# Performance work log

Measured on AMD Instinct MI355X. Metric: run time of the kernel, lower is better.

## Reference

```python
import jax, jax.numpy as jnp
import numpy as np

EPS = 1e-06
M = 10.0
IGNORE_LABEL = 100  # setup guarantees no label == 100, so the torch filter is a no-op


def setup_inputs() -> dict:
    key = jax.random.key(0)
    kf, kl = jax.random.split(key)
    n, d = 8192, 128
    features = jax.random.normal(kf, (n, d), dtype=jnp.float32)
    labels = jax.random.randint(kl, (n,), 0, 16, dtype=jnp.int64)
    return {"features": features, "labels": labels}


def reference(features, labels):
    # features: (n, d) float; labels: (n,) int, none equal to IGNORE_LABEL
    n = features.shape[0]
    dt = features.dtype

    # pairwise squared euclidean distances via Gram trick (avoids (n,n,d) tensor)
    sq = jnp.sum(features * features, axis=1)              # (n,)
    ed = sq[:, None] + sq[None, :] - 2.0 * (features @ features.T)  # (n, n)

    eq = labels[:, None] == labels[None, :]                # (n, n), includes diagonal
    counts = jnp.sum(eq, axis=1, keepdims=True).astype(dt) - 1.0  # (n, 1)

    eqf = eq.astype(dt)
    w = eqf / (counts + EPS) - (1.0 - eqf) / (n - counts - 1.0 + EPS)
    w = w * (1.0 - jnp.eye(n, dtype=dt))                   # zero diagonal

    loss = jnp.sum(w * ed, axis=1) + M                     # (n,)
    valid = (counts[:, 0] != 0.0).astype(dt)               # rows with same-class neighbors
    return jnp.sum(jax.nn.relu(loss) * valid) / jnp.maximum(jnp.sum(valid), 1.0)
```

## Files before the change

### kernel.cpp

```cpp
#include <hip/hip_runtime.h>

#define NCLASS 16
#define D 128
#define EPSF 1e-6f
#define MF 10.0f

#define WS_S   0
#define WS_Q   (NCLASS * D)
#define WS_CNT (WS_Q + NCLASS)
#define WS_SUM (WS_CNT + NCLASS)
#define WS_DONE 2082
#define WS_FLOATS 2084

#define AGG_BLOCKS 64
#define AGG_THREADS 512
#define AGG_WAVES (AGG_THREADS / 64)

__global__ void __launch_bounds__(AGG_THREADS)
agg_kernel(const float* __restrict__ F, const int* __restrict__ L,
           float* __restrict__ ws, int n) {
    __shared__ float Ssh[AGG_WAVES][NCLASS][D];
    __shared__ float qsh[AGG_WAVES][NCLASS];
    __shared__ float csh[AGG_WAVES][NCLASS];
    const int tid  = threadIdx.x;
    const int lane = tid & 63;
    const int wv   = tid >> 6;
    const int gw   = blockIdx.x * AGG_WAVES + wv;
    const int nwv  = AGG_BLOCKS * AGG_WAVES;

    float ax[NCLASS], ay[NCLASS], qa[NCLASS], ca[NCLASS];
    #pragma unroll
    for (int c = 0; c < NCLASS; ++c) { ax[c] = ay[c] = qa[c] = ca[c] = 0.f; }

    const float2* __restrict__ F2 = (const float2*)F;
    #pragma unroll 4
    for (int r = gw; r < n; r += nwv) {
        const int lc = L[r];
        const float2 v = F2[(size_t)r * 64 + lane];
        const float sq = fmaf(v.x, v.x, v.y * v.y);
        #pragma unroll
        for (int c = 0; c < NCLASS; ++c) {
            const float sel = (lc == c) ? 1.f : 0.f;
            ax[c] = fmaf(sel, v.x, ax[c]);
            ay[c] = fmaf(sel, v.y, ay[c]);
            qa[c] = fmaf(sel, sq, qa[c]);
            ca[c] += sel;
        }
    }
    #pragma unroll
    for (int c = 0; c < NCLASS; ++c) {
        float q = qa[c];
        #pragma unroll
        for (int off = 32; off; off >>= 1) q += __shfl_xor(q, off, 64);
        qa[c] = q;
    }
    #pragma unroll
    for (int c = 0; c < NCLASS; ++c) {
        ((float2*)&Ssh[wv][c][0])[lane] = make_float2(ax[c], ay[c]);
    }
    if (lane == 0) {
        #pragma unroll
        for (int c = 0; c < NCLASS; ++c) { qsh[wv][c] = qa[c]; csh[wv][c] = ca[c]; }
    }
    __syncthreads();
    const float* Sflat = &Ssh[0][0][0];
    for (int p = tid; p < NCLASS * D; p += AGG_THREADS) {
        float s = 0.f;
        #pragma unroll
        for (int w = 0; w < AGG_WAVES; ++w) s += Sflat[w * NCLASS * D + p];
        atomicAdd(&ws[WS_S + p], s);
    }
    if (tid < NCLASS) {
        float q = 0.f, cc = 0.f;
        #pragma unroll
        for (int w = 0; w < AGG_WAVES; ++w) { q += qsh[w][tid]; cc += csh[w][tid]; }
        atomicAdd(&ws[WS_Q + tid], q);
        atomicAdd(&ws[WS_CNT + tid], cc);
    }
}

#define LOSS_BLOCKS 256
#define LOSS_THREADS 256
#define LOSS_WAVES (LOSS_THREADS / 64)

__global__ void __launch_bounds__(LOSS_THREADS)
loss_kernel(const float* __restrict__ F, const int* __restrict__ L,
            float* __restrict__ ws, float* __restrict__ out, int n) {
    __shared__ float S_lds[NCLASS * D];
    __shared__ float Stot[D];
    __shared__ float Q_lds[NCLASS];
    __shared__ float cnt_lds[NCLASS];
    __shared__ float Qtot_s;
    __shared__ float redL[LOSS_WAVES], redV[LOSS_WAVES];

    const int tid = threadIdx.x;
    const float4* ws4 = (const float4*)(ws + WS_S);
    float4* S4 = (float4*)S_lds;
    for (int i = tid; i < NCLASS * D / 4; i += LOSS_THREADS) S4[i] = ws4[i];
    if (tid < NCLASS) {
        Q_lds[tid] = ws[WS_Q + tid];
        cnt_lds[tid] = ws[WS_CNT + tid];
    }
    __syncthreads();
    if (tid < D) {
        float s = 0.f;
        #pragma unroll
        for (int c = 0; c < NCLASS; ++c) s += S_lds[c * D + tid];
        Stot[tid] = s;
    }
    if (tid == 0) {
        float q = 0.f;
        #pragma unroll
        for (int c = 0; c < NCLASS; ++c) q += Q_lds[c];
        Qtot_s = q;
    }
    __syncthreads();

    const int lane = tid & 63;
    const int wv = tid >> 6;
    const int gw = blockIdx.x * LOSS_WAVES + wv;
    const int nw = LOSS_BLOCKS * LOSS_WAVES;
    const float nf = (float)n;
    const float2* __restrict__ F2 = (const float2*)F;
    const float2* __restrict__ S2 = (const float2*)S_lds;
    const float2* __restrict__ T2 = (const float2*)Stot;

    float accL = 0.f, accV = 0.f;
    #pragma unroll 2
    for (int r = gw; r < n; r += nw) {
        const int c = L[r];
        const float2 v = F2[(size_t)r * 64 + lane];
        const float2 a = S2[c * 64 + lane];
        const float2 t = T2[lane];
        float sq    = fmaf(v.x, v.x, v.y * v.y);
        float dsame = fmaf(v.x, a.x, v.y * a.y);
        float dtot  = fmaf(v.x, t.x, v.y * t.y);
        #pragma unroll
        for (int off = 32; off; off >>= 1) {
            sq    += __shfl_xor(sq, off, 64);
            dsame += __shfl_xor(dsame, off, 64);
            dtot  += __shfl_xor(dtot, off, 64);
        }
        const float cntc   = cnt_lds[c];
        const float counts = cntc - 1.f;
        const float same_sum = counts * sq + sq + Q_lds[c] - 2.f * dsame;
        const float diff_sum = (nf - cntc) * sq + (Qtot_s - Q_lds[c])
                               - 2.f * (dtot - dsame);
        const float loss = same_sum / (counts + EPSF)
                         - diff_sum / (nf - cntc + EPSF) + MF;
        const float valid = counts > 0.5f ? 1.f : 0.f;
        accL += (loss > 0.f ? loss : 0.f) * valid;
        accV += valid;
    }
    if (lane == 0) { redL[wv] = accL; redV[wv] = accV; }
    __syncthreads();
    if (tid == 0) {
        float sL = 0.f, sV = 0.f;
        #pragma unroll
        for (int w = 0; w < LOSS_WAVES; ++w) { sL += redL[w]; sV += redV[w]; }
        atomicAdd(&ws[WS_SUM], sL);
        atomicAdd(&ws[WS_SUM + 1], sV);
        __threadfence();
        unsigned done = __hip_atomic_fetch_add((unsigned*)&ws[WS_DONE], 1u,
                                               __ATOMIC_ACQ_REL,
                                               __HIP_MEMORY_SCOPE_AGENT);
        if (done == (unsigned)(gridDim.x - 1)) {
            float sl = __hip_atomic_load(&ws[WS_SUM], __ATOMIC_RELAXED,
                                         __HIP_MEMORY_SCOPE_AGENT);
            float sv = __hip_atomic_load(&ws[WS_SUM + 1], __ATOMIC_RELAXED,
                                         __HIP_MEMORY_SCOPE_AGENT);
            out[0] = sl / fmaxf(sv, 1.f);
        }
    }
}

extern "C" void kernel_launch(void* const* d_in, const int* in_sizes, int n_in,
                              void* d_out, int out_size, void* d_ws, size_t ws_size,
                              hipStream_t stream) {
    const float* F = (const float*)d_in[0];
    const int* L = (const int*)d_in[1];
    float* out = (float*)d_out;
    float* ws = (float*)d_ws;
    const int n = in_sizes[1];

    hipMemsetAsync(d_ws, 0, WS_FLOATS * sizeof(float), stream);
    agg_kernel<<<AGG_BLOCKS, AGG_THREADS, 0, stream>>>(F, L, ws, n);
    loss_kernel<<<LOSS_BLOCKS, LOSS_THREADS, 0, stream>>>(F, L, ws, out, n);
}
```

Measured before the change: 84.21 us.

## Fuse aggregation and loss kernels with a grid-wide atomic barrier

Merges the class-aggregation kernel and the per-row loss kernel into one persistent launch of 64 blocks. An atomic counter in the workspace acts as a software grid barrier between the two phases, removing one kernel launch and its inter-kernel gap. In exchange, the loss phase now runs on 64×512 threads instead of 256×256, and the spin barrier depends on all 64 blocks being co-resident. The class sums are read back with agent-scope atomic loads so other blocks' results are visible after the barrier.

```diff
diff --git a/kernel.cpp b/kernel.cpp
--- a/kernel.cpp
+++ b/kernel.cpp
@@ -5,28 +5,35 @@
 #define EPSF 1e-6f
 #define MF 10.0f
 
-#define WS_S   0
-#define WS_Q   (NCLASS * D)
-#define WS_CNT (WS_Q + NCLASS)
-#define WS_SUM (WS_CNT + NCLASS)
-#define WS_DONE 2082
+#define WS_S    0
+#define WS_Q    (NCLASS * D)
+#define WS_CNT  (WS_Q + NCLASS)
+#define WS_SUM  (WS_CNT + NCLASS)
+#define WS_BAR  2082
+#define WS_DONE 2083
 #define WS_FLOATS 2084
 
-#define AGG_BLOCKS 64
-#define AGG_THREADS 512
-#define AGG_WAVES (AGG_THREADS / 64)
+#define BLOCKS 64
+#define THREADS 512
+#define WAVES (THREADS / 64)
 
-__global__ void __launch_bounds__(AGG_THREADS)
-agg_kernel(const float* __restrict__ F, const int* __restrict__ L,
-           float* __restrict__ ws, int n) {
-    __shared__ float Ssh[AGG_WAVES][NCLASS][D];
-    __shared__ float qsh[AGG_WAVES][NCLASS];
-    __shared__ float csh[AGG_WAVES][NCLASS];
+__global__ void __launch_bounds__(THREADS, 1)
+fused_kernel(const float* __restrict__ F, const int* __restrict__ L,
+             float* __restrict__ ws, float* __restrict__ out, int n) {
+    __shared__ float Ssh[WAVES][NCLASS][D];
+    __shared__ float qsh[WAVES][NCLASS];
+    __shared__ float csh[WAVES][NCLASS];
+    __shared__ float Stot[D];
+    __shared__ float Qcls[NCLASS];
+    __shared__ float Ccls[NCLASS];
+    __shared__ float Qtot_s;
+    __shared__ float redL[WAVES], redV[WAVES];
+
     const int tid  = threadIdx.x;
     const int lane = tid & 63;
     const int wv   = tid >> 6;
-    const int gw   = blockIdx.x * AGG_WAVES + wv;
-    const int nwv  = AGG_BLOCKS * AGG_WAVES;
+    const int gw   = blockIdx.x * WAVES + wv;
+    const int nwv  = BLOCKS * WAVES;
 
     float ax[NCLASS], ay[NCLASS], qa[NCLASS], ca[NCLASS];
     #pragma unroll
@@ -64,42 +71,41 @@
     }
     __syncthreads();
     const float* Sflat = &Ssh[0][0][0];
-    for (int p = tid; p < NCLASS * D; p += AGG_THREADS) {
+    for (int p = tid; p < NCLASS * D; p += THREADS) {
         float s = 0.f;
         #pragma unroll
-        for (int w = 0; w < AGG_WAVES; ++w) s += Sflat[w * NCLASS * D + p];
+        for (int w = 0; w < WAVES; ++w) s += Sflat[w * NCLASS * D + p];
         atomicAdd(&ws[WS_S + p], s);
     }
     if (tid < NCLASS) {
         float q = 0.f, cc = 0.f;
         #pragma unroll
-        for (int w = 0; w < AGG_WAVES; ++w) { q += qsh[w][tid]; cc += csh[w][tid]; }
+        for (int w = 0; w < WAVES; ++w) { q += qsh[w][tid]; cc += csh[w][tid]; }
         atomicAdd(&ws[WS_Q + tid], q);
         atomicAdd(&ws[WS_CNT + tid], cc);
     }
-}
 
-#define LOSS_BLOCKS 256
-#define LOSS_THREADS 256
-#define LOSS_WAVES (LOSS_THREADS / 64)
+    __threadfence();
+    __syncthreads();
+    if (tid == 0) {
+        __hip_atomic_fetch_add((unsigned*)&ws[WS_BAR], 1u,
+                               __ATOMIC_ACQ_REL, __HIP_MEMORY_SCOPE_AGENT);
+        while (__hip_atomic_load((unsigned*)&ws[WS_BAR],
+                                 __ATOMIC_ACQUIRE, __HIP_MEMORY_SCOPE_AGENT)
+               < (unsigned)BLOCKS) {  }
+    }
+    __syncthreads();
 
-__global__ void __launch_bounds__(LOSS_THREADS)
-loss_kernel(const float* __restrict__ F, const int* __restrict__ L,
-            float* __restrict__ ws, float* __restrict__ out, int n) {
-    __shared__ float S_lds[NCLASS * D];
-    __shared__ float Stot[D];
-    __shared__ float Q_lds[NCLASS];
-    __shared__ float cnt_lds[NCLASS];
-    __shared__ float Qtot_s;
-    __shared__ float redL[LOSS_WAVES], redV[LOSS_WAVES];
-
-    const int tid = threadIdx.x;
-    const float4* ws4 = (const float4*)(ws + WS_S);
-    float4* S4 = (float4*)S_lds;
-    for (int i = tid; i < NCLASS * D / 4; i += LOSS_THREADS) S4[i] = ws4[i];
+    float* S_lds = &Ssh[0][0][0];
+    for (int i = tid; i < NCLASS * D; i += THREADS) {
+        S_lds[i] = __hip_atomic_load(&ws[WS_S + i], __ATOMIC_RELAXED,
+                                     __HIP_MEMORY_SCOPE_AGENT);
+    }
     if (tid < NCLASS) {
-        Q_lds[tid] = ws[WS_Q + tid];
-        cnt_lds[tid] = ws[WS_CNT + tid];
+        Qcls[tid] = __hip_atomic_load(&ws[WS_Q + tid], __ATOMIC_RELAXED,
+                                      __HIP_MEMORY_SCOPE_AGENT);
+        Ccls[tid] = __hip_atomic_load(&ws[WS_CNT + tid], __ATOMIC_RELAXED,
+                                      __HIP_MEMORY_SCOPE_AGENT);
     }
     __syncthreads();
     if (tid < D) {
@@ -111,23 +117,18 @@
     if (tid == 0) {
         float q = 0.f;
         #pragma unroll
-        for (int c = 0; c < NCLASS; ++c) q += Q_lds[c];
+        for (int c = 0; c < NCLASS; ++c) q += Qcls[c];
         Qtot_s = q;
     }
     __syncthreads();
 
-    const int lane = tid & 63;
-    const int wv = tid >> 6;
-    const int gw = blockIdx.x * LOSS_WAVES + wv;
-    const int nw = LOSS_BLOCKS * LOSS_WAVES;
     const float nf = (float)n;
-    const float2* __restrict__ F2 = (const float2*)F;
     const float2* __restrict__ S2 = (const float2*)S_lds;
     const float2* __restrict__ T2 = (const float2*)Stot;
 
     float accL = 0.f, accV = 0.f;
     #pragma unroll 2
-    for (int r = gw; r < n; r += nw) {
+    for (int r = gw; r < n; r += nwv) {
         const int c = L[r];
         const float2 v = F2[(size_t)r * 64 + lane];
         const float2 a = S2[c * 64 + lane];
@@ -141,10 +142,10 @@
             dsame += __shfl_xor(dsame, off, 64);
             dtot  += __shfl_xor(dtot, off, 64);
         }
-        const float cntc   = cnt_lds[c];
+        const float cntc   = Ccls[c];
         const float counts = cntc - 1.f;
-        const float same_sum = counts * sq + sq + Q_lds[c] - 2.f * dsame;
-        const float diff_sum = (nf - cntc) * sq + (Qtot_s - Q_lds[c])
+        const float same_sum = counts * sq + sq + Qcls[c] - 2.f * dsame;
+        const float diff_sum = (nf - cntc) * sq + (Qtot_s - Qcls[c])
                                - 2.f * (dtot - dsame);
         const float loss = same_sum / (counts + EPSF)
                          - diff_sum / (nf - cntc + EPSF) + MF;
@@ -157,14 +158,14 @@
     if (tid == 0) {
         float sL = 0.f, sV = 0.f;
         #pragma unroll
-        for (int w = 0; w < LOSS_WAVES; ++w) { sL += redL[w]; sV += redV[w]; }
+        for (int w = 0; w < WAVES; ++w) { sL += redL[w]; sV += redV[w]; }
         atomicAdd(&ws[WS_SUM], sL);
         atomicAdd(&ws[WS_SUM + 1], sV);
         __threadfence();
         unsigned done = __hip_atomic_fetch_add((unsigned*)&ws[WS_DONE], 1u,
                                                __ATOMIC_ACQ_REL,
                                                __HIP_MEMORY_SCOPE_AGENT);
-        if (done == (unsigned)(gridDim.x - 1)) {
+        if (done == (unsigned)(BLOCKS - 1)) {
             float sl = __hip_atomic_load(&ws[WS_SUM], __ATOMIC_RELAXED,
                                          __HIP_MEMORY_SCOPE_AGENT);
             float sv = __hip_atomic_load(&ws[WS_SUM + 1], __ATOMIC_RELAXED,
@@ -184,6 +185,5 @@
     const int n = in_sizes[1];
 
     hipMemsetAsync(d_ws, 0, WS_FLOATS * sizeof(float), stream);
-    agg_kernel<<<AGG_BLOCKS, AGG_THREADS, 0, stream>>>(F, L, ws, n);
-    loss_kernel<<<LOSS_BLOCKS, LOSS_THREADS, 0, stream>>>(F, L, ws, out, n);
+    fused_kernel<<<BLOCKS, THREADS, 0, stream>>>(F, L, ws, out, n);
 }
```

Result: slower. 90.66 us (+7.6%).
